# Performance work log

Hardware: AMD Instinct MI355X
Metric: run time of the kernel (lower is better)

## Reference

```python
import jax, jax.numpy as jnp
import numpy as np

N, D, K = 500000, 256, 64

def setup_inputs() -> dict:
    key = jax.random.key(0)
    kq, km = jax.random.split(key)
    query = jax.random.normal(kq, (D,), dtype=jnp.float32)
    mat = jax.random.normal(km, (N, D), dtype=jnp.float32)
    return {"query": query, "mat": mat, "k": K}

def reference(query, mat, k):
    # scores = mat @ query  : [N]
    scores = jnp.einsum("nd,d->n", mat, query)
    # top-k selection over all stored vectors
    _, idx = jax.lax.top_k(scores, k)
    # gather the selected rows : [k, D]
    out = jnp.take(mat, idx, axis=0)
    # idx stands in for the metadata gather (meta[i] for i in idx)
    return out, idx
```

## Files before the change

### kernel.cpp

```cpp
#include <hip/hip_runtime.h>
#include <stdint.h>

#define DIM 256
#define TOPK 64
#define HIST_BINS 65536
#define CAP 4096

__device__ __forceinline__ uint32_t fkey(float f) {
  uint32_t u = __float_as_uint(f);
  return (u & 0x80000000u) ? ~u : (u | 0x80000000u);
}

__global__ __launch_bounds__(256) void score_kernel(
    const float* __restrict__ mat, const float* __restrict__ query,
    float* __restrict__ scores, uint32_t* __restrict__ hist,
    int* __restrict__ cnt, int n) {
  int tid = blockIdx.x * 256 + threadIdx.x;
  if (tid < HIST_BINS) hist[tid] = 0u;
  if (tid == 0) *cnt = 0;

  int wave = tid >> 6;
  int lane = threadIdx.x & 63;
  if (wave < n) {
    float4 q = ((const float4*)query)[lane];
    float4 m = ((const float4*)(mat + (size_t)wave * DIM))[lane];
    float d = m.x * q.x + m.y * q.y + m.z * q.z + m.w * q.w;
#pragma unroll
    for (int off = 32; off > 0; off >>= 1) d += __shfl_xor(d, off, 64);
    if (lane == 0) scores[wave] = d;
  }
}

__global__ __launch_bounds__(256) void hist_kernel(
    const float* __restrict__ scores, uint32_t* __restrict__ hist, int n) {
  int i = blockIdx.x * 256 + threadIdx.x;
  int stride = gridDim.x * 256;
  for (; i < n; i += stride) {
    atomicAdd(&hist[fkey(scores[i]) >> 16], 1u);
  }
}

__global__ __launch_bounds__(256) void thresh_kernel(
    const uint32_t* __restrict__ hist, int* __restrict__ tbin) {
  __shared__ uint32_t s[256];
  __shared__ int fc;
  __shared__ uint32_t above;
  int t = threadIdx.x;

  uint32_t acc = 0;
  const uint4* h4 = (const uint4*)(hist + t * 256);
  for (int j = 0; j < 64; ++j) {
    uint4 v = h4[j];
    acc += v.x + v.y + v.z + v.w;
  }
  s[t] = acc;
  __syncthreads();
  for (int off = 1; off < 256; off <<= 1) {
    uint32_t v = (t + off < 256) ? s[t + off] : 0u;
    __syncthreads();
    s[t] += v;
    __syncthreads();
  }
  if (s[t] >= TOPK && (t == 255 || s[t + 1] < TOPK)) {
    fc = t;
    above = (t == 255) ? 0u : s[t + 1];
  }
  __syncthreads();
  int c = fc;
  uint32_t a = above;
  uint32_t h = hist[c * 256 + t];
  __syncthreads();
  s[t] = h;
  __syncthreads();
  for (int off = 1; off < 256; off <<= 1) {
    uint32_t v = (t + off < 256) ? s[t + off] : 0u;
    __syncthreads();
    s[t] += v;
    __syncthreads();
  }
  if (a + s[t] >= TOPK && (t == 255 || a + s[t + 1] < TOPK)) {
    *tbin = c * 256 + t;
  }
}

__global__ __launch_bounds__(256) void collect_kernel(
    const float* __restrict__ scores, const int* __restrict__ tbin,
    int* __restrict__ cnt, unsigned long long* __restrict__ cand, int n) {
  uint32_t T = (uint32_t)(*tbin);
  int i = blockIdx.x * 256 + threadIdx.x;
  int stride = gridDim.x * 256;
  for (; i < n; i += stride) {
    uint32_t key = fkey(scores[i]);
    if ((key >> 16) >= T) {
      int pos = atomicAdd(cnt, 1);
      if (pos < CAP) {
        cand[pos] = ((unsigned long long)key << 32) | (uint32_t)(~(uint32_t)i);
      }
    }
  }
}

__global__ __launch_bounds__(256) void final_kernel(
    const unsigned long long* __restrict__ cand, const int* __restrict__ cnt,
    const float* __restrict__ mat, float* __restrict__ out) {
  __shared__ unsigned long long c[CAP];
  __shared__ int sel[TOPK];
  int t = threadIdx.x;
  int M = *cnt;
  if (M > CAP) M = CAP;

  for (int i = t; i < M; i += 256) c[i] = cand[i];
  __syncthreads();

  for (int i = t; i < M; i += 256) {
    unsigned long long mykey = c[i];
    int rank = 0;
    for (int j = 0; j < M; ++j) rank += (c[j] > mykey) ? 1 : 0;
    if (rank < TOPK) sel[rank] = (int)(~(uint32_t)(mykey & 0xFFFFFFFFull));
  }
  __syncthreads();

  if (t < TOPK) out[TOPK * DIM + t] = (float)sel[t];

  int wv = t >> 6, lane = t & 63;
  for (int r = wv; r < TOPK; r += 4) {
    size_t row = (size_t)sel[r];
    float4 v = ((const float4*)(mat + row * DIM))[lane];
    ((float4*)(out + r * DIM))[lane] = v;
  }
}

extern "C" void kernel_launch(void* const* d_in, const int* in_sizes, int n_in,
                              void* d_out, int out_size, void* d_ws, size_t ws_size,
                              hipStream_t stream) {
  const float* query = (const float*)d_in[0];
  const float* mat = (const float*)d_in[1];
  float* out = (float*)d_out;
  int n = in_sizes[1] / DIM;

  char* ws = (char*)d_ws;
  float* scores = (float*)ws;
  uint32_t* hist = (uint32_t*)(ws + (2u << 20));
  int* tbin = (int*)(ws + (2u << 20) + HIST_BINS * 4);
  int* cnt = tbin + 1;
  unsigned long long* cand =
      (unsigned long long*)(ws + (2u << 20) + HIST_BINS * 4 + 16);

  int sblocks = (n + 3) / 4;
  score_kernel<<<sblocks, 256, 0, stream>>>(mat, query, scores, hist, cnt, n);
  hist_kernel<<<512, 256, 0, stream>>>(scores, hist, n);
  thresh_kernel<<<1, 256, 0, stream>>>(hist, tbin);
  collect_kernel<<<512, 256, 0, stream>>>(scores, tbin, cnt, cand, n);
  final_kernel<<<1, 256, 0, stream>>>(cand, cnt, mat, out);
}
```

Baseline: 799.1 us.

## Fuse histogram into score kernel, two rows per wave, nontemporal loads

Moves the histogram atomicAdd into the score kernel, so the separate histogram pass and its re-read of scores are gone. Each wave now handles two rows, with 32 lanes per row loading two float4s, which halves the wave count and shortens the shuffle reduction. Matrix loads use nontemporal hints to avoid polluting the cache. Histogram zeroing moves to a separate small kernel that must finish first, adding a launch. Atomics are now spread across the bandwidth-bound scoring pass, which risks contention.

Measured after the change: 803.1 us. About the same (+0.5%).

```diff
diff --git a/kernel.cpp b/kernel.cpp
--- a/kernel.cpp
+++ b/kernel.cpp
@@ -6,37 +6,44 @@
 #define HIST_BINS 65536
 #define CAP 4096
 
+typedef float nfloat4 __attribute__((ext_vector_type(4)));
+
 __device__ __forceinline__ uint32_t fkey(float f) {
   uint32_t u = __float_as_uint(f);
   return (u & 0x80000000u) ? ~u : (u | 0x80000000u);
 }
 
+__global__ __launch_bounds__(256) void zero_kernel(uint32_t* __restrict__ hist,
+                                                   int* __restrict__ cnt) {
+  int tid = blockIdx.x * 256 + threadIdx.x;
+  ((uint4*)hist)[tid] = make_uint4(0u, 0u, 0u, 0u);
+  if (tid == 0) *cnt = 0;
+}
+
 __global__ __launch_bounds__(256) void score_kernel(
     const float* __restrict__ mat, const float* __restrict__ query,
-    float* __restrict__ scores, uint32_t* __restrict__ hist,
-    int* __restrict__ cnt, int n) {
-  int tid = blockIdx.x * 256 + threadIdx.x;
-  if (tid < HIST_BINS) hist[tid] = 0u;
-  if (tid == 0) *cnt = 0;
+    float* __restrict__ scores, uint32_t* __restrict__ hist, int n) {
+  int wave = (blockIdx.x * 256 + threadIdx.x) >> 6;
+  int lane = threadIdx.x & 63;
+  int half = lane >> 5;
+  int sub = lane & 31;
+  int row = 2 * wave + half;
+  if (row >= n) return;
 
-  int wave = tid >> 6;
-  int lane = threadIdx.x & 63;
-  if (wave < n) {
-    float4 q = ((const float4*)query)[lane];
-    float4 m = ((const float4*)(mat + (size_t)wave * DIM))[lane];
-    float d = m.x * q.x + m.y * q.y + m.z * q.z + m.w * q.w;
+  const nfloat4* rp = (const nfloat4*)(mat + (size_t)row * DIM);
+  nfloat4 m0 = __builtin_nontemporal_load(rp + sub);
+  nfloat4 m1 = __builtin_nontemporal_load(rp + sub + 32);
+  float4 q0 = ((const float4*)query)[sub];
+  float4 q1 = ((const float4*)query)[sub + 32];
+
+  float d = m0.x * q0.x + m0.y * q0.y + m0.z * q0.z + m0.w * q0.w +
+            m1.x * q1.x + m1.y * q1.y + m1.z * q1.z + m1.w * q1.w;
 #pragma unroll
-    for (int off = 32; off > 0; off >>= 1) d += __shfl_xor(d, off, 64);
-    if (lane == 0) scores[wave] = d;
-  }
-}
+  for (int off = 16; off > 0; off >>= 1) d += __shfl_xor(d, off, 64);
 
-__global__ __launch_bounds__(256) void hist_kernel(
-    const float* __restrict__ scores, uint32_t* __restrict__ hist, int n) {
-  int i = blockIdx.x * 256 + threadIdx.x;
-  int stride = gridDim.x * 256;
-  for (; i < n; i += stride) {
-    atomicAdd(&hist[fkey(scores[i]) >> 16], 1u);
+  if (sub == 0) {
+    scores[row] = d;
+    atomicAdd(&hist[fkey(d) >> 16], 1u);
   }
 }
 
@@ -146,9 +153,10 @@
   unsigned long long* cand =
       (unsigned long long*)(ws + (2u << 20) + HIST_BINS * 4 + 16);
 
-  int sblocks = (n + 3) / 4;
-  score_kernel<<<sblocks, 256, 0, stream>>>(mat, query, scores, hist, cnt, n);
-  hist_kernel<<<512, 256, 0, stream>>>(scores, hist, n);
+  zero_kernel<<<64, 256, 0, stream>>>(hist, cnt);
+  int waves = (n + 1) / 2;
+  int sblocks = (waves + 3) / 4;
+  score_kernel<<<sblocks, 256, 0, stream>>>(mat, query, scores, hist, n);
   thresh_kernel<<<1, 256, 0, stream>>>(hist, tbin);
   collect_kernel<<<512, 256, 0, stream>>>(scores, tbin, cnt, cand, n);
   final_kernel<<<1, 256, 0, stream>>>(cand, cnt, mat, out);
```
